# Kernel tuning notes

Measured on AMD Instinct MI355X. Metric: run time of the kernel, lower is better.

Reference implementation:

```python
import jax, jax.numpy as jnp
import numpy as np

B, L, D, H, UNITS = 64, 1024, 1024, 1024, 1024


def setup_inputs() -> dict:
    key = jax.random.key(0)
    ks = jax.random.split(key, 8)
    s = lambda fan_in: 1.0 / np.sqrt(fan_in)
    return {
        "features": jax.random.normal(ks[0], (B, L, D), jnp.float32),
        "hidden": jax.random.normal(ks[1], (B, H), jnp.float32),
        "W1": jax.random.normal(ks[2], (D, UNITS), jnp.float32) * s(D),
        "b1": jnp.zeros((UNITS,), jnp.float32),
        "W2": jax.random.normal(ks[3], (H, UNITS), jnp.float32) * s(H),
        "b2": jnp.zeros((UNITS,), jnp.float32),
        "V": jax.random.normal(ks[4], (UNITS, 1), jnp.float32) * s(UNITS),
        "bV": jnp.zeros((1,), jnp.float32),
    }


def reference(features, hidden, W1, b1, W2, b2, V, bV):
    # features: [B, L, D], hidden: [B, H]
    proj_f = jnp.einsum("bld,du->blu", features, W1) + b1          # [B, L, U]
    proj_h = (hidden @ W2 + b2)[:, None, :]                         # [B, 1, U]
    score = jnp.tanh(proj_f + proj_h)                               # [B, L, U]
    logits = jnp.einsum("blu,uo->blo", score, V) + bV               # [B, L, 1]
    attention_weights = jax.nn.softmax(logits, axis=1)              # [B, L, 1]
    context_vector = jnp.sum(attention_weights * features, axis=1)  # [B, D]
    return context_vector, attention_weights
```

## Files before the change

kernel.cpp:

```cpp
#include <hip/hip_runtime.h>
#include <hip/hip_bf16.h>
#include <stdint.h>

#define B_ 64
#define L_ 1024
#define D_ 1024
#define U_ 1024
#define M_ (B_ * L_)

typedef __attribute__((ext_vector_type(8))) __bf16 bf16x8;
typedef __attribute__((ext_vector_type(4))) float f32x4;

__device__ __forceinline__ unsigned short f2bf(float f) {
  unsigned u = __float_as_uint(f);
  unsigned r = (u + 0x7fffu + ((u >> 16) & 1u)) >> 16;
  return (unsigned short)r;
}

__device__ __forceinline__ float bf2f(unsigned short h) {
  return __uint_as_float(((unsigned)h) << 16);
}

__device__ __forceinline__ void async_copy16(const void* gptr, void* ldsptr) {
  __builtin_amdgcn_global_load_lds(
      (const __attribute__((address_space(1))) void*)gptr,
      (__attribute__((address_space(3))) void*)ldsptr,
      16, 0, 0);
}

__global__ __launch_bounds__(256) void convert_f_bf16(
    const float4* __restrict__ src, uint4* __restrict__ dst) {
  const long n8 = (long)M_ * D_ / 8;
  for (long i = (long)blockIdx.x * 256 + threadIdx.x; i < n8;
       i += (long)gridDim.x * 256) {
    float4 x = src[2 * i];
    float4 y = src[2 * i + 1];
    uint4 o;
    o.x = (unsigned)f2bf(x.x) | ((unsigned)f2bf(x.y) << 16);
    o.y = (unsigned)f2bf(x.z) | ((unsigned)f2bf(x.w) << 16);
    o.z = (unsigned)f2bf(y.x) | ((unsigned)f2bf(y.y) << 16);
    o.w = (unsigned)f2bf(y.z) | ((unsigned)f2bf(y.w) << 16);
    dst[i] = o;
  }
}

__global__ __launch_bounds__(256) void transpose_w1(
    const float* __restrict__ W1, unsigned short* __restrict__ W1T) {
  __shared__ float tile[32][33];
  int tx = threadIdx.x & 31, ty = threadIdx.x >> 5;
  int u0 = blockIdx.x * 32, k0 = blockIdx.y * 32;
#pragma unroll
  for (int i = ty; i < 32; i += 8) tile[i][tx] = W1[(long)(k0 + i) * U_ + u0 + tx];
  __syncthreads();
#pragma unroll
  for (int i = ty; i < 32; i += 8) {
    int u = u0 + i, k = k0 + tx;
    W1T[(long)u * D_ + k] = f2bf(tile[tx][i]);
  }
}

__global__ __launch_bounds__(256) void proj_h_kernel(
    const float* __restrict__ hidden, const float* __restrict__ W2,
    const float* __restrict__ b1, const float* __restrict__ b2,
    float* __restrict__ ph) {
  int u = blockIdx.x * 256 + threadIdx.x;
  int bbase = blockIdx.y * 8;
  int h0 = blockIdx.z * 128;
  float acc[8];
  float bias = (blockIdx.z == 0) ? (b1[u] + b2[u]) : 0.0f;
#pragma unroll
  for (int i = 0; i < 8; ++i) acc[i] = bias;
  for (int h = h0; h < h0 + 128; ++h) {
    float w = W2[(long)h * U_ + u];
#pragma unroll
    for (int i = 0; i < 8; ++i) acc[i] += hidden[(bbase + i) * 1024 + h] * w;
  }
#pragma unroll
  for (int i = 0; i < 8; ++i) atomicAdd(&ph[(bbase + i) * U_ + u], acc[i]);
}

#define LDA(rb, i) (*(const bf16x8*)&S[(rb) + arow + (i)*512])
#define LDB(rb, j) (*(const bf16x8*)&S[(rb) + 8192 + brow + (j)*512])
#define MMA(i, j)                                                    \
  acc[i][j] = __builtin_amdgcn_mfma_f32_16x16x32_bf16(a0f[i], bff[j], \
                                                      acc[i][j], 0, 0, 0)
#define MMB(i, j)                                                        \
  acc[4 + i][j] = __builtin_amdgcn_mfma_f32_16x16x32_bf16(               \
      a1f[i], bff[j], acc[4 + i][j], 0, 0, 0)
#define SYNC_MAIN \
  asm volatile("s_waitcnt vmcnt(4)" ::: "memory"); __builtin_amdgcn_s_barrier()
#define SYNC_LAST \
  asm volatile("s_waitcnt vmcnt(0)" ::: "memory"); __builtin_amdgcn_s_barrier()
#define SYNC_NONE ((void)0)

#define WINDOW(WT, DO_STAGE, ENDSYNC)                                          \
  {                                                                            \
    const int rb = ((WT) & 3) << 14;                                           \
    const int sb = (((WT) + 2) & 3) << 14;                                     \
    const int sk = ((WT) + 2) << 5;                                            \
    bf16x8 a0f[4], a1f[4], bff[4];                                             \
                 \
    if (DO_STAGE) {                                                            \
      async_copy16(a0 + sk, &S[sb + (wave << 9)]);                             \
      async_copy16(a1 + sk, &S[sb + 4096 + (wave << 9)]);                      \
      async_copy16(b0 + sk, &S[sb + 8192 + (wave << 9)]);                      \
      async_copy16(b1 + sk, &S[sb + 12288 + (wave << 9)]);                     \
    }                                                                          \
       \
    a0f[0] = LDA(rb, 0); a0f[1] = LDA(rb, 1);                                  \
    a0f[2] = LDA(rb, 2); a0f[3] = LDA(rb, 3);                                  \
    bff[0] = LDB(rb, 0); bff[1] = LDB(rb, 1);                                  \
    bff[2] = LDB(rb, 2); bff[3] = LDB(rb, 3);                                  \
    a1f[0] = LDA(rb, 4); a1f[1] = LDA(rb, 5);                                  \
    a1f[2] = LDA(rb, 6); a1f[3] = LDA(rb, 7);                                  \
          \
    asm volatile("s_waitcnt lgkmcnt(4)" ::: "memory");                         \
    __builtin_amdgcn_sched_barrier(0);                                         \
    __builtin_amdgcn_s_setprio(1);                                             \
    MMA(0, 0); MMA(0, 1); MMA(0, 2); MMA(0, 3);                                \
    MMA(1, 0); MMA(1, 1); MMA(1, 2); MMA(1, 3);                                \
    MMA(2, 0); MMA(2, 1); MMA(2, 2); MMA(2, 3);                                \
    MMA(3, 0); MMA(3, 1); MMA(3, 2); MMA(3, 3);                                \
    __builtin_amdgcn_s_setprio(0);                                             \
    asm volatile("s_waitcnt lgkmcnt(0)" ::: "memory");                         \
    __builtin_amdgcn_sched_barrier(0);                                         \
    __builtin_amdgcn_s_setprio(1);                                             \
    MMB(0, 0); MMB(0, 1); MMB(0, 2); MMB(0, 3);                                \
    MMB(1, 0); MMB(1, 1); MMB(1, 2); MMB(1, 3);                                \
    MMB(2, 0); MMB(2, 1); MMB(2, 2); MMB(2, 3);                                \
    MMB(3, 0); MMB(3, 1); MMB(3, 2); MMB(3, 3);                                \
    __builtin_amdgcn_s_setprio(0);                                             \
    ENDSYNC;                                                                   \
  }

__global__ __launch_bounds__(512, 2) void fused_score_kernel(
    const unsigned short* __restrict__ A,
    const unsigned short* __restrict__ Bt,
    const float* __restrict__ ph,
    const float* __restrict__ V,
    float* __restrict__ logits) {
  __shared__ unsigned short S[65536];

  const int tid = threadIdx.x;
  const int wave = tid >> 6;
  const int lane = tid & 63;
  const int l15 = lane & 15;
  const int quad = lane >> 4;
  const int wm = wave >> 2;
  const int wn = wave & 3;

  const int bid = blockIdx.x;
  const int wg = (bid & 7) * 128 + (bid >> 3);
  const int mtile = wg >> 2;
  const int ntile = wg & 3;
  const long m0 = (long)mtile * 256;
  const int n0 = ntile * 256;

  const int srow = (wave << 4) + (lane >> 2);
  const int skel = ((lane & 3) << 3) ^ ((lane & 32) ? 16 : 0);
  const unsigned short* a0 = A + (m0 + srow) * 1024 + skel;
  const unsigned short* a1 = A + (m0 + 128 + srow) * 1024 + skel;
  const unsigned short* b0 = Bt + ((long)n0 + srow) * 1024 + skel;
  const unsigned short* b1 = Bt + ((long)n0 + 128 + srow) * 1024 + skel;

  const int xorq = ((quad * 8) ^ ((l15 & 8) << 1));
  const int arow = (wm * 128 + l15) * 32 + xorq;
  const int brow = (wn * 64 + l15) * 32 + xorq;

  f32x4 acc[8][4];
#pragma unroll
  for (int i = 0; i < 8; ++i)
#pragma unroll
    for (int j = 0; j < 4; ++j) acc[i][j] = (f32x4){0.f, 0.f, 0.f, 0.f};

#pragma unroll
  for (int t = 0; t < 2; ++t) {
    const int sbase = t << 14;
    async_copy16(a0 + t * 32, &S[sbase + (wave << 9)]);
    async_copy16(a1 + t * 32, &S[sbase + 4096 + (wave << 9)]);
    async_copy16(b0 + t * 32, &S[sbase + 8192 + (wave << 9)]);
    async_copy16(b1 + t * 32, &S[sbase + 12288 + (wave << 9)]);
  }
  asm volatile("s_waitcnt vmcnt(4)" ::: "memory");
  __builtin_amdgcn_s_barrier();

#pragma unroll 1
  for (int t = 0; t < 30; ++t) {
    WINDOW(t, 1, SYNC_MAIN)
  }
  WINDOW(30, 0, SYNC_LAST)
  WINDOW(31, 0, SYNC_NONE)

  const int b = (int)(m0 >> 10);
  float phv[4], vv[4];
#pragma unroll
  for (int j = 0; j < 4; ++j) {
    int u = n0 + wn * 64 + j * 16 + l15;
    phv[j] = ph[b * U_ + u];
    vv[j] = V[u];
  }
#pragma unroll
  for (int i = 0; i < 8; ++i) {
#pragma unroll
    for (int r = 0; r < 4; ++r) {
      float part = 0.f;
#pragma unroll
      for (int j = 0; j < 4; ++j) {
        float s = acc[i][j][r] + phv[j];
        float e = __expf(2.0f * s);
        float th = 1.0f - 2.0f * __builtin_amdgcn_rcpf(e + 1.0f);
        part += th * vv[j];
      }
      part += __shfl_xor(part, 1, 16);
      part += __shfl_xor(part, 2, 16);
      part += __shfl_xor(part, 4, 16);
      part += __shfl_xor(part, 8, 16);
      if (l15 == 0)
        atomicAdd(&logits[m0 + wm * 128 + i * 16 + quad * 4 + r], part);
    }
  }
}

__global__ __launch_bounds__(256) void softmax_kernel(
    const float* __restrict__ logits, float* __restrict__ wout) {
  __shared__ float redm[4];
  __shared__ float reds[4];
  int b = blockIdx.x;
  int tid = threadIdx.x;
  int wave = tid >> 6, lane = tid & 63;
  float4 v = *(const float4*)&logits[b * 1024 + tid * 4];
  float m = fmaxf(fmaxf(v.x, v.y), fmaxf(v.z, v.w));
#pragma unroll
  for (int off = 32; off >= 1; off >>= 1) m = fmaxf(m, __shfl_xor(m, off, 64));
  if (lane == 0) redm[wave] = m;
  __syncthreads();
  m = fmaxf(fmaxf(redm[0], redm[1]), fmaxf(redm[2], redm[3]));
  float e0 = __expf(v.x - m), e1 = __expf(v.y - m);
  float e2 = __expf(v.z - m), e3 = __expf(v.w - m);
  float s = e0 + e1 + e2 + e3;
#pragma unroll
  for (int off = 32; off >= 1; off >>= 1) s += __shfl_xor(s, off, 64);
  if (lane == 0) reds[wave] = s;
  __syncthreads();
  s = reds[0] + reds[1] + reds[2] + reds[3];
  float inv = 1.0f / s;
  float4 o = {e0 * inv, e1 * inv, e2 * inv, e3 * inv};
  *(float4*)&wout[b * 1024 + tid * 4] = o;
}

__global__ __launch_bounds__(256) void context_kernel(
    const unsigned short* __restrict__ Fh, const float* __restrict__ wv,
    float* __restrict__ out) {
  int b = blockIdx.x;
  int d4 = threadIdx.x * 4;
  int l0 = blockIdx.y * 128;
  const unsigned short* fp = Fh + ((long)b * 1024 + l0) * 1024;
  const float* wp = wv + b * 1024 + l0;
  float a0 = 0.f, a1 = 0.f, a2 = 0.f, a3 = 0.f;
#pragma unroll 4
  for (int l = 0; l < 128; ++l) {
    ushort4 f = *(const ushort4*)(fp + (long)l * 1024 + d4);
    float w = wp[l];
    a0 += w * bf2f(f.x);
    a1 += w * bf2f(f.y);
    a2 += w * bf2f(f.z);
    a3 += w * bf2f(f.w);
  }
  atomicAdd(&out[b * 1024 + d4 + 0], a0);
  atomicAdd(&out[b * 1024 + d4 + 1], a1);
  atomicAdd(&out[b * 1024 + d4 + 2], a2);
  atomicAdd(&out[b * 1024 + d4 + 3], a3);
}

extern "C" void kernel_launch(void* const* d_in, const int* in_sizes, int n_in,
                              void* d_out, int out_size, void* d_ws, size_t ws_size,
                              hipStream_t stream) {
  const float* features = (const float*)d_in[0];
  const float* hidden   = (const float*)d_in[1];
  const float* W1       = (const float*)d_in[2];
  const float* b1       = (const float*)d_in[3];
  const float* W2       = (const float*)d_in[4];
  const float* b2       = (const float*)d_in[5];
  const float* V        = (const float*)d_in[6];

  char* ws = (char*)d_ws;
  unsigned short* Fh  = (unsigned short*)ws;
  unsigned short* W1T = (unsigned short*)(ws + 134217728);
  float* ph     = (float*)(ws + 134217728 + 2097152);
  float* logits = (float*)(ws + 134217728 + 2097152 + 262144);
  float* ctx  = (float*)d_out;
  float* wout = (float*)d_out + 65536;

  hipMemsetAsync(ph, 0, 262144 + 262144, stream);
  hipMemsetAsync(d_out, 0, 65536 * sizeof(float), stream);

  convert_f_bf16<<<4096, 256, 0, stream>>>((const float4*)features, (uint4*)Fh);
  transpose_w1<<<dim3(32, 32), 256, 0, stream>>>(W1, W1T);
  proj_h_kernel<<<dim3(4, 8, 8), 256, 0, stream>>>(hidden, W2, b1, b2, ph);
  fused_score_kernel<<<1024, 512, 0, stream>>>(Fh, W1T, ph, V, logits);
  softmax_kernel<<<64, 256, 0, stream>>>(logits, wout);
  context_kernel<<<dim3(64, 8), 256, 0, stream>>>(Fh, wout, ctx);
}
```

Before: 612.9 us.

## Load B fragments directly from global into registers, halving LDS staging

The B (weight) tile no longer goes through the LDS ring buffer. Each wave reads its MFMA B fragments straight from global memory into registers at the start of each K window. Only the A tile is staged asynchronously in LDS, which halves shared memory use and could let two workgroups share a CU. The workgroup barrier now runs every second window instead of every window. In exchange, global-load latency sits on the critical path of each window, and waves that share B columns fetch the same B data redundantly.

```diff
diff --git a/kernel.cpp b/kernel.cpp
--- a/kernel.cpp
+++ b/kernel.cpp
@@ -80,40 +80,37 @@
 }
 
 #define LDA(rb, i) (*(const bf16x8*)&S[(rb) + arow + (i)*512])
-#define LDB(rb, j) (*(const bf16x8*)&S[(rb) + 8192 + brow + (j)*512])
 #define MMA(i, j)                                                    \
   acc[i][j] = __builtin_amdgcn_mfma_f32_16x16x32_bf16(a0f[i], bff[j], \
                                                       acc[i][j], 0, 0, 0)
 #define MMB(i, j)                                                        \
   acc[4 + i][j] = __builtin_amdgcn_mfma_f32_16x16x32_bf16(               \
       a1f[i], bff[j], acc[4 + i][j], 0, 0, 0)
-#define SYNC_MAIN \
-  asm volatile("s_waitcnt vmcnt(4)" ::: "memory"); __builtin_amdgcn_s_barrier()
-#define SYNC_LAST \
+#define SYNC_BAR \
   asm volatile("s_waitcnt vmcnt(0)" ::: "memory"); __builtin_amdgcn_s_barrier()
 #define SYNC_NONE ((void)0)
 
-#define WINDOW(WT, DO_STAGE, ENDSYNC)                                          \
+#define WINDOW(WT, DO_STAGE, BV, ENDSYNC)                                      \
   {                                                                            \
-    const int rb = ((WT) & 3) << 14;                                           \
-    const int sb = (((WT) + 2) & 3) << 14;                                     \
+    const int rb = ((WT) & 3) << 13;                                           \
+    const int sb = (((WT) + 2) & 3) << 13;                                     \
     const int sk = ((WT) + 2) << 5;                                            \
+    const int kof = (WT) << 5;                                                 \
     bf16x8 a0f[4], a1f[4], bff[4];                                             \
-                 \
+      \
+    bff[0] = *(const bf16x8*)(bp + kof);                                       \
+    bff[1] = *(const bf16x8*)(bp + kof + 16384);                               \
+    bff[2] = *(const bf16x8*)(bp + kof + 32768);                               \
+    bff[3] = *(const bf16x8*)(bp + kof + 49152);                               \
     if (DO_STAGE) {                                                            \
       async_copy16(a0 + sk, &S[sb + (wave << 9)]);                             \
       async_copy16(a1 + sk, &S[sb + 4096 + (wave << 9)]);                      \
-      async_copy16(b0 + sk, &S[sb + 8192 + (wave << 9)]);                      \
-      async_copy16(b1 + sk, &S[sb + 12288 + (wave << 9)]);                     \
     }                                                                          \
-       \
     a0f[0] = LDA(rb, 0); a0f[1] = LDA(rb, 1);                                  \
     a0f[2] = LDA(rb, 2); a0f[3] = LDA(rb, 3);                                  \
-    bff[0] = LDB(rb, 0); bff[1] = LDB(rb, 1);                                  \
-    bff[2] = LDB(rb, 2); bff[3] = LDB(rb, 3);                                  \
     a1f[0] = LDA(rb, 4); a1f[1] = LDA(rb, 5);                                  \
     a1f[2] = LDA(rb, 6); a1f[3] = LDA(rb, 7);                                  \
-          \
+    asm volatile("s_waitcnt vmcnt(" #BV ")" ::: "memory");                     \
     asm volatile("s_waitcnt lgkmcnt(4)" ::: "memory");                         \
     __builtin_amdgcn_sched_barrier(0);                                         \
     __builtin_amdgcn_s_setprio(1);                                             \
@@ -139,7 +136,7 @@
     const float* __restrict__ ph,
     const float* __restrict__ V,
     float* __restrict__ logits) {
-  __shared__ unsigned short S[65536];
+  __shared__ unsigned short S[32768];
 
   const int tid = threadIdx.x;
   const int wave = tid >> 6;
@@ -160,12 +157,12 @@
   const int skel = ((lane & 3) << 3) ^ ((lane & 32) ? 16 : 0);
   const unsigned short* a0 = A + (m0 + srow) * 1024 + skel;
   const unsigned short* a1 = A + (m0 + 128 + srow) * 1024 + skel;
-  const unsigned short* b0 = Bt + ((long)n0 + srow) * 1024 + skel;
-  const unsigned short* b1 = Bt + ((long)n0 + 128 + srow) * 1024 + skel;
+
+  const unsigned short* bp =
+      Bt + ((long)(n0 + wn * 64 + l15)) * 1024 + quad * 8;
 
   const int xorq = ((quad * 8) ^ ((l15 & 8) << 1));
   const int arow = (wm * 128 + l15) * 32 + xorq;
-  const int brow = (wn * 64 + l15) * 32 + xorq;
 
   f32x4 acc[8][4];
 #pragma unroll
@@ -175,21 +172,21 @@
 
 #pragma unroll
   for (int t = 0; t < 2; ++t) {
-    const int sbase = t << 14;
+    const int sbase = t << 13;
     async_copy16(a0 + t * 32, &S[sbase + (wave << 9)]);
     async_copy16(a1 + t * 32, &S[sbase + 4096 + (wave << 9)]);
-    async_copy16(b0 + t * 32, &S[sbase + 8192 + (wave << 9)]);
-    async_copy16(b1 + t * 32, &S[sbase + 12288 + (wave << 9)]);
-  }
-  asm volatile("s_waitcnt vmcnt(4)" ::: "memory");
+  }
+  asm volatile("s_waitcnt vmcnt(0)" ::: "memory");
   __builtin_amdgcn_s_barrier();
 
 #pragma unroll 1
-  for (int t = 0; t < 30; ++t) {
-    WINDOW(t, 1, SYNC_MAIN)
-  }
-  WINDOW(30, 0, SYNC_LAST)
-  WINDOW(31, 0, SYNC_NONE)
+  for (int j = 0; j < 15; ++j) {
+    const int t0 = 2 * j;
+    WINDOW(t0, 1, 2, SYNC_NONE)
+    WINDOW(t0 + 1, 1, 2, SYNC_BAR)
+  }
+  WINDOW(30, 0, 0, SYNC_NONE)
+  WINDOW(31, 0, 0, SYNC_NONE)
 
   const int b = (int)(m0 >> 10);
   float phv[4], vv[4];
```

Result: slower. 682.3 us (+11.3%).
